# Performance work log

Hardware: AMD Instinct MI355X
Metric: run time of the kernel (lower is better)

## Reference

```python
import jax, jax.numpy as jnp
import numpy as np

B, L, H, E = 16, 4096, 3, 512   # q: [B, L, H, E]; in_channels = H*E = 1536
M = 128                          # number of selected frequency modes
F_LEN = L // 2 + 1               # rfft length


def setup_inputs() -> dict:
    key = jax.random.key(0)
    kq, kr, ki = jax.random.split(key, 3)
    q = jax.random.normal(kq, (B, L, H, E), dtype=jnp.float32)
    # get_frequency_modes('random'): shuffle range(L//2), take M, sort (distinct modes)
    rng = np.random.default_rng(0)
    index = jnp.asarray(np.sort(rng.permutation(L // 2)[:M]).astype(np.int32))
    # torch.rand on cfloat samples real & imag uniform[0,1); scale = 1/(in*out)
    scale = 1.0 / float((H * E) * (H * E))
    w_real = scale * jax.random.uniform(kr, (H, E, E, M), dtype=jnp.float32)
    w_imag = scale * jax.random.uniform(ki, (H, E, E, M), dtype=jnp.float32)
    return {"q": q, "w_real": w_real, "w_imag": w_imag, "index": index, "mask": 0}


def reference(q, w_real, w_imag, index, mask):
    # mask is unused by FourierBlock.forward (matches original)
    w = (w_real + 1j * w_imag).astype(jnp.complex64)      # [H, E_in, E_out, M]
    x = jnp.transpose(q, (0, 2, 3, 1))                    # [B, H, E, L]
    x_ft = jnp.fft.rfft(x, axis=-1)                       # [B, H, E, F_LEN] complex64
    # gather selected modes, batched complex matmul over all modes at once
    x_sel = x_ft[..., index]                              # [B, H, E_in, M]
    out_sel = jnp.einsum('bhim,hiom->bhom', x_sel, w)     # [B, H, E_out, M]
    # scatter back into zero-initialized spectrum
    out_ft = jnp.zeros((B, H, E, F_LEN), dtype=jnp.complex64).at[..., index].set(out_sel)
    x_out = jnp.fft.irfft(out_ft, n=L, axis=-1)           # [B, H, E, L] float32
    return x_out
```

## Files before the change

kernel.cpp:

```cpp
#include <hip/hip_runtime.h>
#include <hip/hip_bf16.h>


#define L_TOT 4096

typedef __attribute__((ext_vector_type(4))) float f32x4;
typedef __attribute__((ext_vector_type(2))) float f32x2;
typedef __attribute__((ext_vector_type(2))) unsigned u32x2;
typedef __attribute__((ext_vector_type(8))) short s16x8;
typedef __attribute__((ext_vector_type(4))) unsigned short u16x4;

__device__ __forceinline__ unsigned short f2bf(float f) {
    unsigned u = __builtin_bit_cast(unsigned, f);
    u = (u + 0x7fffu + ((u >> 16) & 1u)) >> 16;
    return (unsigned short)u;
}

__device__ __forceinline__ void gload_lds16(const void* g, void* l) {
    __builtin_amdgcn_global_load_lds((const __attribute__((address_space(1))) void*)g,
                                     (__attribute__((address_space(3))) void*)l,
                                     16, 0, 0);
}

__global__ __launch_bounds__(256) void build_ta(const int* __restrict__ index,
                                                unsigned short* __restrict__ T_A) {
    const int idx = blockIdx.x * 256 + threadIdx.x;
    const int m2 = idx >> 12;
    const int l  = idx & (L_TOT - 1);
    const int k  = index[m2 >> 1];
    const int tt = (k * l) & (L_TOT - 1);
    const float x = (float)tt * (1.0f / 2048.0f);
    T_A[idx] = f2bf((m2 & 1) ? -sinpif(x) : cospif(x));
}

__global__ __launch_bounds__(256) void build_tc(const int* __restrict__ index,
                                                unsigned short* __restrict__ T_C) {
    const int idx = blockIdx.x * 256 + threadIdx.x;
    const int l  = idx >> 8;
    const int m2 = idx & 255;
    const int k  = index[m2 >> 1];
    const int tt = (k * l) & (L_TOT - 1);
    const float x = (float)tt * (1.0f / 2048.0f);
    const float s = (k == 0 ? 1.0f : 2.0f) * (1.0f / (float)L_TOT);
    T_C[idx] = f2bf(s * ((m2 & 1) ? -sinpif(x) : cospif(x)));
}

__global__ __launch_bounds__(256) void gemm_a(const float* __restrict__ q,
                                              const unsigned short* __restrict__ T_A,
                                              unsigned short* __restrict__ Xbf) {
    __shared__ unsigned short As[64 * 64];
    __shared__ unsigned short Bs[256 * 64];

    const int bid = blockIdx.x;
    const int b   = bid / 24;
    const int cht = bid % 24;
    const int ch0 = cht * 64;
    const int h   = ch0 >> 9;
    const int i0  = ch0 & 511;
    const int t   = threadIdx.x;
    const int lane = t & 63;
    const int w    = t >> 6;
    const int chq  = t & 15;
    const int lg   = t >> 4;

    const float* qb = q + (size_t)b * L_TOT * 1536 + ch0 + chq * 4;

    f32x4 acc[4][4];
#pragma unroll
    for (int mi = 0; mi < 4; ++mi)
#pragma unroll
        for (int ni = 0; ni < 4; ++ni) acc[mi][ni] = (f32x4)0.0f;

    for (int kt = 0; kt < L_TOT; kt += 64) {
        __syncthreads();
#pragma unroll
        for (int p = 0; p < 8; ++p) {
            const int u = p * 256 + t;
            const int row = u >> 3, c16 = u & 7;
            const unsigned short* src = T_A + (size_t)row * L_TOT + kt + ((c16 ^ (row & 7)) * 8);
            unsigned short* dst = Bs + (size_t)(p * 256 + w * 64) * 8;
            gload_lds16(src, dst);
        }
        f32x4 v[4];
#pragma unroll
        for (int r = 0; r < 4; ++r)
            v[r] = *reinterpret_cast<const f32x4*>(qb + (size_t)(kt + lg * 4 + r) * 1536);
#pragma unroll
        for (int j = 0; j < 4; ++j) {
            const int c = chq * 4 + j;
            uint2 pk;
            pk.x = f2bf(v[0][j]) | ((unsigned)f2bf(v[1][j]) << 16);
            pk.y = f2bf(v[2][j]) | ((unsigned)f2bf(v[3][j]) << 16);
            *reinterpret_cast<uint2*>(As + c * 64 + ((lg * 4) ^ ((c & 7) << 3))) = pk;
        }
        __syncthreads();

#pragma unroll
        for (int kk = 0; kk < 2; ++kk) {
            const int c16 = kk * 4 + (lane >> 4);
            s16x8 af[4], bfr[4];
#pragma unroll
            for (int mi = 0; mi < 4; ++mi) {
                const int row = mi * 16 + (lane & 15);
                af[mi] = *reinterpret_cast<const s16x8*>(As + row * 64 + ((c16 ^ (row & 7)) * 8));
            }
#pragma unroll
            for (int ni = 0; ni < 4; ++ni) {
                const int row = w * 64 + ni * 16 + (lane & 15);
                bfr[ni] = *reinterpret_cast<const s16x8*>(Bs + row * 64 + ((c16 ^ (row & 7)) * 8));
            }
#pragma unroll
            for (int mi = 0; mi < 4; ++mi)
#pragma unroll
                for (int ni = 0; ni < 4; ++ni)
                    acc[mi][ni] = __builtin_amdgcn_mfma_f32_16x16x32_bf16(af[mi], bfr[ni], acc[mi][ni], 0, 0, 0);
        }
    }

    const size_t cbase = (((size_t)h * 16 + b) * 512 + i0) * 256;
#pragma unroll
    for (int mi = 0; mi < 4; ++mi) {
        const int r0 = mi * 16 + (lane >> 4) * 4;
#pragma unroll
        for (int ni = 0; ni < 4; ++ni) {
            const int col = w * 64 + ni * 16 + (lane & 15);
#pragma unroll
            for (int j = 0; j < 4; ++j)
                Xbf[cbase + (size_t)(r0 + j) * 256 + col] = f2bf(acc[mi][ni][j]);
        }
    }
}

template <int MODE>
__global__ __launch_bounds__(256) void gemm_bf16(const unsigned short* __restrict__ A,
                                                 const unsigned short* __restrict__ Bt,
                                                 void* __restrict__ Cv) {
    constexpr int BM   = 128;
    constexpr int BK   = 64;
    constexpr int KTOT = 256;
    constexpr int LDAB = 256;
    constexpr int LDC  = 4096;
    constexpr int MFR  = BM / 32;
    constexpr int APASS = BM * 8 / 256;
    constexpr int BPASS = 4;

    __shared__ unsigned short As[BM * BK];
    __shared__ unsigned short Bs[128 * BK];

    const int t = threadIdx.x;
    const int lane = t & 63;
    const int w = t >> 6;
    const int wr = w >> 1, wc = w & 1;

    const int mt = blockIdx.x >> 5, nt = blockIdx.x & 31;
    const unsigned short* Ab = A + (size_t)mt * 128 * 256;
    const unsigned short* Bb = Bt + (size_t)nt * 128 * 256;
    const size_t cbase = (size_t)mt * 128 * 4096 + nt * 128;

    f32x4 acc[MFR][4];
#pragma unroll
    for (int mi = 0; mi < MFR; ++mi)
#pragma unroll
        for (int ni = 0; ni < 4; ++ni) acc[mi][ni] = (f32x4)0.0f;

    for (int kt = 0; kt < KTOT; kt += BK) {
        __syncthreads();
#pragma unroll
        for (int p = 0; p < APASS; ++p) {
            const int u = p * 256 + t;
            const int row = u >> 3, c16 = u & 7;
            const unsigned short* src = Ab + (size_t)row * LDAB + kt + ((c16 ^ (row & 7)) * 8);
            unsigned short* dst = As + (size_t)(p * 256 + w * 64) * 8;
            gload_lds16(src, dst);
        }
#pragma unroll
        for (int p = 0; p < BPASS; ++p) {
            const int u = p * 256 + t;
            const int row = u >> 3, c16 = u & 7;
            const unsigned short* src = Bb + (size_t)row * LDAB + kt + ((c16 ^ (row & 7)) * 8);
            unsigned short* dst = Bs + (size_t)(p * 256 + w * 64) * 8;
            gload_lds16(src, dst);
        }
        __syncthreads();

#pragma unroll
        for (int kk = 0; kk < 2; ++kk) {
            const int c16 = kk * 4 + (lane >> 4);
            s16x8 af[MFR], bfr[4];
#pragma unroll
            for (int mi = 0; mi < MFR; ++mi) {
                const int row = wr * (BM / 2) + mi * 16 + (lane & 15);
                af[mi] = *reinterpret_cast<const s16x8*>(As + row * BK + ((c16 ^ (row & 7)) * 8));
            }
#pragma unroll
            for (int ni = 0; ni < 4; ++ni) {
                const int row = wc * 64 + ni * 16 + (lane & 15);
                bfr[ni] = *reinterpret_cast<const s16x8*>(Bs + row * BK + ((c16 ^ (row & 7)) * 8));
            }
#pragma unroll
            for (int mi = 0; mi < MFR; ++mi)
#pragma unroll
                for (int ni = 0; ni < 4; ++ni)
                    acc[mi][ni] = __builtin_amdgcn_mfma_f32_16x16x32_bf16(af[mi], bfr[ni], acc[mi][ni], 0, 0, 0);
        }
    }

#pragma unroll
    for (int mi = 0; mi < MFR; ++mi) {
        const int r0 = wr * (BM / 2) + mi * 16 + (lane >> 4) * 4;
#pragma unroll
        for (int ni = 0; ni < 4; ++ni) {
            const int col = wc * 64 + ni * 16 + (lane & 15);
#pragma unroll
            for (int j = 0; j < 4; ++j)
                ((float*)Cv)[cbase + (size_t)(r0 + j) * LDC + col] = acc[mi][ni][j];
        }
    }
}

#define SB_STAGE(BUF, IB)                                                      \
    _Pragma("unroll")                                                          \
    for (int pp = 0; pp < 2; ++pp) {                                           \
        const int u = pp * 256 + t;                                            \
        const int row = u >> 5;                                                \
        const int col = u & 31;                                                \
        const int ii = row >> 2, oo = row & 3;                                 \
        const size_t goff = (size_t)((IB) + ii) * 65536 + oo * 128 + col * 4;  \
        gload_lds16(wr_base + goff, (char*)&Wl[BUF][0][0][0][0] + (size_t)u * 16); \
        gload_lds16(wi_base + goff, (char*)&Wl[BUF][1][0][0][0] + (size_t)u * 16); \
    }

__global__ __launch_bounds__(256, 3) void stage_b(const unsigned short* __restrict__ Xbf,
                                                  const float* __restrict__ wr,
                                                  const float* __restrict__ wi,
                                                  unsigned short* __restrict__ Y0,
                                                  unsigned short* __restrict__ P1) {
    __shared__ float Wl[2][2][4][4][128];
    const int bid = blockIdx.x;
    const int ic  = bid / 384;
    const int g   = bid % 384;
    const int h   = g >> 7;
    const int ot  = g & 127;
    const int t    = threadIdx.x;
    const int lane = t & 63;
    const int w    = t >> 6;
    const int b0   = w * 4;
    const int o0   = ot * 4;
    const int i_lo = ic * 256;

    const float* wr_base = wr + (size_t)h * 33554432 + (size_t)o0 * 128;
    const float* wi_base = wi + (size_t)h * 33554432 + (size_t)o0 * 128;
    const unsigned short* x0 = Xbf + (size_t)(h * 16 + b0) * 512 * 256 + lane * 4;

    float aR[4][4][2], aI[4][4][2];
#pragma unroll
    for (int bb = 0; bb < 4; ++bb)
#pragma unroll
        for (int oo = 0; oo < 4; ++oo) {
            aR[bb][oo][0] = aR[bb][oo][1] = 0.f;
            aI[bb][oo][0] = aI[bb][oo][1] = 0.f;
        }

    SB_STAGE(0, i_lo);

#pragma unroll 1
    for (int c = 0; c < 64; ++c) {
        const int ib = i_lo + c * 4;
        const int p  = c & 1;
        __builtin_amdgcn_sched_barrier(0);
        u32x2 xv[4][4];
#pragma unroll
        for (int i = 0; i < 4; ++i)
#pragma unroll
            for (int bb = 0; bb < 4; ++bb)
                xv[i][bb] = *reinterpret_cast<const u32x2*>(
                    x0 + (size_t)bb * 131072 + (size_t)(ib + i) * 256);
        __builtin_amdgcn_sched_barrier(0);
        const int ibn = (c + 1 < 64) ? (ib + 4) : i_lo;
        if (p == 0) { SB_STAGE(1, ibn); } else { SB_STAGE(0, ibn); }
        __builtin_amdgcn_sched_barrier(0);
        asm volatile("s_waitcnt vmcnt(20)" ::: "memory");
        __builtin_amdgcn_sched_barrier(0);
        __builtin_amdgcn_s_barrier();
        __builtin_amdgcn_sched_barrier(0);
#pragma unroll
        for (int i = 0; i < 4; ++i) {
            f32x2 wrv[4], wiv[4];
#pragma unroll
            for (int oo = 0; oo < 4; ++oo) {
                wrv[oo] = *reinterpret_cast<const f32x2*>(&Wl[p][0][i][oo][lane * 2]);
                wiv[oo] = *reinterpret_cast<const f32x2*>(&Wl[p][1][i][oo][lane * 2]);
            }
#pragma unroll
            for (int bb = 0; bb < 4; ++bb) {
                float xr[2], xi[2];
#pragma unroll
                for (int mm = 0; mm < 2; ++mm) {
                    const unsigned xu = xv[i][bb][mm];
                    xr[mm] = __builtin_bit_cast(float, xu << 16);
                    xi[mm] = __builtin_bit_cast(float, xu & 0xffff0000u);
                }
#pragma unroll
                for (int oo = 0; oo < 4; ++oo)
#pragma unroll
                    for (int mm = 0; mm < 2; ++mm) {
                        const float wrj = wrv[oo][mm];
                        const float wij = wiv[oo][mm];
                        aR[bb][oo][mm] = fmaf(xr[mm], wrj, aR[bb][oo][mm]);
                        aR[bb][oo][mm] = fmaf(-xi[mm], wij, aR[bb][oo][mm]);
                        aI[bb][oo][mm] = fmaf(xr[mm], wij, aI[bb][oo][mm]);
                        aI[bb][oo][mm] = fmaf(xi[mm], wrj, aI[bb][oo][mm]);
                    }
            }
        }
        __builtin_amdgcn_sched_barrier(0);
        __builtin_amdgcn_s_barrier();
    }

    unsigned short* yout = ic ? P1 : Y0;
#pragma unroll
    for (int bb = 0; bb < 4; ++bb)
#pragma unroll
        for (int oo = 0; oo < 4; ++oo) {
            const size_t row = ((size_t)(b0 + bb) * 3 + h) * 512 + o0 + oo;
            u32x2 pk;
            pk.x = f2bf(aR[bb][oo][0]) | ((unsigned)f2bf(aI[bb][oo][0]) << 16);
            pk.y = f2bf(aR[bb][oo][1]) | ((unsigned)f2bf(aI[bb][oo][1]) << 16);
            *reinterpret_cast<u32x2*>(reinterpret_cast<char*>(yout) + row * 512 + lane * 8) = pk;
        }
}

__global__ __launch_bounds__(256) void reduce_y(unsigned short* __restrict__ Ybf,
                                                const unsigned short* __restrict__ P1) {
    const int idx = blockIdx.x * 256 + threadIdx.x;
    const uint4 a = reinterpret_cast<const uint4*>(Ybf)[idx];
    const uint4 b = reinterpret_cast<const uint4*>(P1)[idx];
    const unsigned av[4] = {a.x, a.y, a.z, a.w};
    const unsigned bv[4] = {b.x, b.y, b.z, b.w};
    unsigned rv[4];
#pragma unroll
    for (int j = 0; j < 4; ++j) {
        const float xr = __builtin_bit_cast(float, av[j] << 16);
        const float xi = __builtin_bit_cast(float, av[j] & 0xffff0000u);
        const float yr = __builtin_bit_cast(float, bv[j] << 16);
        const float yi = __builtin_bit_cast(float, bv[j] & 0xffff0000u);
        rv[j] = f2bf(xr + yr) | ((unsigned)f2bf(xi + yi) << 16);
    }
    uint4 r;
    r.x = rv[0]; r.y = rv[1]; r.z = rv[2]; r.w = rv[3];
    reinterpret_cast<uint4*>(Ybf)[idx] = r;
}

extern "C" void kernel_launch(void* const* d_in, const int* in_sizes, int n_in,
                              void* d_out, int out_size, void* d_ws, size_t ws_size,
                              hipStream_t stream) {
    const float* q     = (const float*)d_in[0];
    const float* w_re  = (const float*)d_in[1];
    const float* w_im  = (const float*)d_in[2];
    const int*   index = (const int*)d_in[3];

    char* ws = (char*)d_ws;
    unsigned short* Xbf = (unsigned short*)(ws);
    unsigned short* P1  = (unsigned short*)(ws + 12582912);
    unsigned short* Ybf = (unsigned short*)(ws + 25165824);
    unsigned short* T_A = (unsigned short*)(ws + 37748736);
    unsigned short* T_C = (unsigned short*)(ws + 39845888);

    build_ta<<<4096, 256, 0, stream>>>(index, T_A);
    build_tc<<<4096, 256, 0, stream>>>(index, T_C);
    gemm_a<<<384, 256, 0, stream>>>(q, T_A, Xbf);
    stage_b<<<768, 256, 0, stream>>>(Xbf, w_re, w_im, Ybf, P1);
    reduce_y<<<3072, 256, 0, stream>>>(Ybf, P1);
    gemm_bf16<1><<<6144, 256, 0, stream>>>(Ybf, T_C, (void*)d_out);
}
```

Before: 478.1 us.

## Software-pipeline X register loads one chunk ahead in stage_b with unroll-by-two

Unrolls the stage_b main loop by two with double-buffered X register tiles (xvA/xvB), so X for the next chunk is loaded while the current chunk computes. W LDS staging is issued right after the barrier following compute, two chunks ahead. This hides global load latency of X behind FMA work, at the cost of extra VGPRs (a second 16x u32x2 buffer), which may hurt occupancy at 3 waves/SIMD. The vmcnt(20) wait count is kept unchanged despite the reordered issue, which may make the wait under- or over-conservative.

```diff
diff --git a/kernel.cpp b/kernel.cpp
--- a/kernel.cpp
+++ b/kernel.cpp
@@ -224,10 +224,50 @@
         const int u = pp * 256 + t;                                            \
         const int row = u >> 5;                                                \
         const int col = u & 31;                                                \
-        const int ii = row >> 2, oo = row & 3;                                 \
-        const size_t goff = (size_t)((IB) + ii) * 65536 + oo * 128 + col * 4;  \
+        const int ii = row >> 2, oo2 = row & 3;                                \
+        const size_t goff = (size_t)((IB) + ii) * 65536 + oo2 * 128 + col * 4; \
         gload_lds16(wr_base + goff, (char*)&Wl[BUF][0][0][0][0] + (size_t)u * 16); \
         gload_lds16(wi_base + goff, (char*)&Wl[BUF][1][0][0][0] + (size_t)u * 16); \
+    }
+
+#define SB_LDX(XV, IB)                                                         \
+    _Pragma("unroll")                                                          \
+    for (int i_ = 0; i_ < 4; ++i_)                                             \
+        _Pragma("unroll")                                                      \
+        for (int bb_ = 0; bb_ < 4; ++bb_)                                      \
+            XV[i_][bb_] = *reinterpret_cast<const u32x2*>(                     \
+                x0 + (size_t)bb_ * 131072 + (size_t)((IB) + i_) * 256);
+
+#define SB_COMP(BUF, XV)                                                       \
+    _Pragma("unroll")                                                          \
+    for (int i = 0; i < 4; ++i) {                                              \
+        f32x2 wrv[4], wiv[4];                                                  \
+        _Pragma("unroll")                                                      \
+        for (int oo = 0; oo < 4; ++oo) {                                       \
+            wrv[oo] = *reinterpret_cast<const f32x2*>(&Wl[BUF][0][i][oo][lane * 2]); \
+            wiv[oo] = *reinterpret_cast<const f32x2*>(&Wl[BUF][1][i][oo][lane * 2]); \
+        }                                                                      \
+        _Pragma("unroll")                                                      \
+        for (int bb = 0; bb < 4; ++bb) {                                       \
+            float xr[2], xi[2];                                                \
+            _Pragma("unroll")                                                  \
+            for (int mm = 0; mm < 2; ++mm) {                                   \
+                const unsigned xu = XV[i][bb][mm];                             \
+                xr[mm] = __builtin_bit_cast(float, xu << 16);                  \
+                xi[mm] = __builtin_bit_cast(float, xu & 0xffff0000u);          \
+            }                                                                  \
+            _Pragma("unroll")                                                  \
+            for (int oo = 0; oo < 4; ++oo)                                     \
+                _Pragma("unroll")                                              \
+                for (int mm = 0; mm < 2; ++mm) {                               \
+                    const float wrj = wrv[oo][mm];                             \
+                    const float wij = wiv[oo][mm];                             \
+                    aR[bb][oo][mm] = fmaf(xr[mm], wrj, aR[bb][oo][mm]);        \
+                    aR[bb][oo][mm] = fmaf(-xi[mm], wij, aR[bb][oo][mm]);       \
+                    aI[bb][oo][mm] = fmaf(xr[mm], wij, aI[bb][oo][mm]);        \
+                    aI[bb][oo][mm] = fmaf(xi[mm], wrj, aI[bb][oo][mm]);        \
+                }                                                              \
+        }                                                                      \
     }
 
 __global__ __launch_bounds__(256, 3) void stage_b(const unsigned short* __restrict__ Xbf,
@@ -261,60 +301,48 @@
             aI[bb][oo][0] = aI[bb][oo][1] = 0.f;
         }
 
+    u32x2 xvA[4][4], xvB[4][4];
+
     SB_STAGE(0, i_lo);
+    SB_LDX(xvA, i_lo);
+    SB_STAGE(1, i_lo + 4);
 
 #pragma unroll 1
-    for (int c = 0; c < 64; ++c) {
-        const int ib = i_lo + c * 4;
-        const int p  = c & 1;
-        __builtin_amdgcn_sched_barrier(0);
-        u32x2 xv[4][4];
-#pragma unroll
-        for (int i = 0; i < 4; ++i)
-#pragma unroll
-            for (int bb = 0; bb < 4; ++bb)
-                xv[i][bb] = *reinterpret_cast<const u32x2*>(
-                    x0 + (size_t)bb * 131072 + (size_t)(ib + i) * 256);
-        __builtin_amdgcn_sched_barrier(0);
-        const int ibn = (c + 1 < 64) ? (ib + 4) : i_lo;
-        if (p == 0) { SB_STAGE(1, ibn); } else { SB_STAGE(0, ibn); }
+    for (int cc = 0; cc < 32; ++cc) {
+        const int c0 = cc * 2;
+        const int ib0 = i_lo + c0 * 4;
+        __builtin_amdgcn_sched_barrier(0);
+        SB_LDX(xvB, ib0 + 4);
         __builtin_amdgcn_sched_barrier(0);
         asm volatile("s_waitcnt vmcnt(20)" ::: "memory");
         __builtin_amdgcn_sched_barrier(0);
         __builtin_amdgcn_s_barrier();
         __builtin_amdgcn_sched_barrier(0);
-#pragma unroll
-        for (int i = 0; i < 4; ++i) {
-            f32x2 wrv[4], wiv[4];
-#pragma unroll
-            for (int oo = 0; oo < 4; ++oo) {
-                wrv[oo] = *reinterpret_cast<const f32x2*>(&Wl[p][0][i][oo][lane * 2]);
-                wiv[oo] = *reinterpret_cast<const f32x2*>(&Wl[p][1][i][oo][lane * 2]);
-            }
-#pragma unroll
-            for (int bb = 0; bb < 4; ++bb) {
-                float xr[2], xi[2];
-#pragma unroll
-                for (int mm = 0; mm < 2; ++mm) {
-                    const unsigned xu = xv[i][bb][mm];
-                    xr[mm] = __builtin_bit_cast(float, xu << 16);
-                    xi[mm] = __builtin_bit_cast(float, xu & 0xffff0000u);
-                }
-#pragma unroll
-                for (int oo = 0; oo < 4; ++oo)
-#pragma unroll
-                    for (int mm = 0; mm < 2; ++mm) {
-                        const float wrj = wrv[oo][mm];
-                        const float wij = wiv[oo][mm];
-                        aR[bb][oo][mm] = fmaf(xr[mm], wrj, aR[bb][oo][mm]);
-                        aR[bb][oo][mm] = fmaf(-xi[mm], wij, aR[bb][oo][mm]);
-                        aI[bb][oo][mm] = fmaf(xr[mm], wij, aI[bb][oo][mm]);
-                        aI[bb][oo][mm] = fmaf(xi[mm], wrj, aI[bb][oo][mm]);
-                    }
-            }
-        }
+        SB_COMP(0, xvA);
         __builtin_amdgcn_sched_barrier(0);
         __builtin_amdgcn_s_barrier();
+        {
+            const int ibs = (c0 + 2 < 64) ? (ib0 + 8) : i_lo;
+            SB_STAGE(0, ibs);
+        }
+        const int ib1 = ib0 + 4;
+        __builtin_amdgcn_sched_barrier(0);
+        {
+            const int ibx = (c0 + 2 < 64) ? (ib1 + 4) : i_lo;
+            SB_LDX(xvA, ibx);
+        }
+        __builtin_amdgcn_sched_barrier(0);
+        asm volatile("s_waitcnt vmcnt(20)" ::: "memory");
+        __builtin_amdgcn_sched_barrier(0);
+        __builtin_amdgcn_s_barrier();
+        __builtin_amdgcn_sched_barrier(0);
+        SB_COMP(1, xvB);
+        __builtin_amdgcn_sched_barrier(0);
+        __builtin_amdgcn_s_barrier();
+        {
+            const int ibs = (c0 + 3 < 64) ? (ib1 + 8) : i_lo;
+            SB_STAGE(1, ibs);
+        }
     }
 
     unsigned short* yout = ic ? P1 : Y0;
```

New measurement: 1.396 ms. 2.92x slower.
